# Optimization experiments

Hardware: AMD Instinct MI355X
Metric: run time of the kernel (lower is better)

## Reference

```python
import jax, jax.numpy as jnp
import numpy as np

B, D, P = 1024, 1024, 16  # batch, latent_dim(=out_dim), part_dim

def setup_inputs() -> dict:
    key = jax.random.key(0)
    k1, k2 = jax.random.split(key)
    x = jax.random.normal(k1, (B, D, P), dtype=jnp.float32)
    # per-part Linear weights, torch Linear weight shape [out, in] stacked over parts
    W = jax.random.normal(k2, (P, D, D), dtype=jnp.float32) * 0.02
    return {"x": x, "W": W}

def reference(x, W):
    # x: [B, D, P]; W: [P, O, D] (O == D here). stack_dim=-1: slice last dim,
    # apply part-specific Linear (no bias) + exact GELU, stack on last dim.
    y = jnp.einsum('bdp,pod->bop', x, W)  # grouped per-part GEMM -> [B, O, P]
    return jax.nn.gelu(y, approximate=False)
```

## Files before the change

### kernel.cpp

```cpp
#include <hip/hip_runtime.h>
#include <hip/hip_bf16.h>
#include <math.h>

typedef __hip_bfloat16 bf16;
typedef __attribute__((ext_vector_type(8))) short bf16x8;
typedef __attribute__((ext_vector_type(4))) float f32x4;

#define DI static __device__ __forceinline__

constexpr int NB = 1024;
constexpr int ND = 1024;
constexpr int NP = 16;
constexpr int BKT = 32;
constexpr int NKT = ND / BKT;
constexpr int LDP = 1032;

DI float gelu_exact(float x) {
    return 0.5f * x * (1.0f + erff(x * 0.70710678118654752f));
}

DI ushort bf16_bits(float f) {
    bf16 h = __float2bfloat16(f);
    return *reinterpret_cast<ushort*>(&h);
}

__global__ __launch_bounds__(256) void pack_kernel(const float* __restrict__ x,
                                                   const float* __restrict__ w,
                                                   bf16* __restrict__ xp,
                                                   bf16* __restrict__ wp) {
    __shared__ ushort lds[16][LDP];
    if (blockIdx.x < NB) {
        const int b = blockIdx.x;
        const int t = threadIdx.x;
        const float* xb = x + (size_t)b * (ND * NP);
#pragma unroll
        for (int it = 0; it < 8; ++it) {
            const int u  = it * 256 + t;
            const int dh = u >> 2;
            const int p0 = (u & 3) * 4;
            const float4 va = *reinterpret_cast<const float4*>(&xb[(size_t)(dh * 2)     * NP + p0]);
            const float4 vb = *reinterpret_cast<const float4*>(&xb[(size_t)(dh * 2 + 1) * NP + p0]);
            const float a0[4] = { va.x, va.y, va.z, va.w };
            const float a1[4] = { vb.x, vb.y, vb.z, vb.w };
#pragma unroll
            for (int k = 0; k < 4; ++k) {
                const uint packed = (uint)bf16_bits(a0[k]) | ((uint)bf16_bits(a1[k]) << 16);
                *reinterpret_cast<uint*>(&lds[p0 + k][dh * 2]) = packed;
            }
        }
        __syncthreads();
        const int p = threadIdx.x >> 4, j = threadIdx.x & 15;
        bf16* dst = xp + (size_t)p * (NB * ND) + (size_t)b * ND;
#pragma unroll
        for (int it = 0; it < 8; ++it) {
            const int c = it * 16 + j;
            *reinterpret_cast<bf16x8*>(&dst[c * 8]) =
                *reinterpret_cast<const bf16x8*>(&lds[p][c * 8]);
        }
    } else {
        const size_t i = ((size_t)(blockIdx.x - NB) * 256 + threadIdx.x) * 8;
        const float4 f0 = *reinterpret_cast<const float4*>(&w[i]);
        const float4 f1 = *reinterpret_cast<const float4*>(&w[i + 4]);
        alignas(16) bf16 tmp[8] = { __float2bfloat16(f0.x), __float2bfloat16(f0.y),
                                    __float2bfloat16(f0.z), __float2bfloat16(f0.w),
                                    __float2bfloat16(f1.x), __float2bfloat16(f1.y),
                                    __float2bfloat16(f1.z), __float2bfloat16(f1.w) };
        *reinterpret_cast<bf16x8*>(&wp[i]) = *reinterpret_cast<const bf16x8*>(tmp);
    }
}

__global__ __launch_bounds__(512, 2) void gemm8_kernel(const bf16* __restrict__ xp,
                                                       const bf16* __restrict__ wp,
                                                       bf16* __restrict__ y) {
    __shared__ bf16 As[3][256 * BKT];
    __shared__ bf16 Bs[3][256 * BKT];
    const int i = blockIdx.x;
    const int p    = ((i & 7) << 1) | ((i >> 3) & 1);
    const int tile = i >> 4;
    const int bt = (tile >> 2) * 256;
    const int ot = (tile & 3) * 256;
    const bf16* A  = xp + (size_t)p * NB * ND;
    const bf16* Bm = wp + (size_t)p * ND * ND;
    const int t = threadIdx.x;
    const int l = t & 63, w = t >> 6;
    const int wr = w >> 2, wc = w & 3;
    const int lr = l & 15, g = l >> 4;

    f32x4 acc[8][4] = {};

    auto stage = [&](int buf, int kt, int q) {
        const int s   = ((q & 1) * 8 + w) * 64 + l;
        const int row = s >> 2;
        const int cb  = (s & 3) ^ (row & 3);
        const bf16* gsrc = (q < 2 ? A + (size_t)(bt + row) * ND
                                  : Bm + (size_t)(ot + row) * ND) + kt * BKT + cb * 8;
        bf16* ldst = (q < 2 ? &As[buf][((q & 1) * 8 + w) * 512]
                            : &Bs[buf][((q & 1) * 8 + w) * 512]);
        __builtin_amdgcn_global_load_lds((const __attribute__((address_space(1))) void*)gsrc,
                                         (__attribute__((address_space(3))) void*)ldst, 16, 0, 0);
    };
    auto readA = [&](int buf, int m) -> bf16x8 {
        const int row  = wr * 128 + m * 16 + lr;
        const int slot = row * 4 + (g ^ (row & 3));
        return *reinterpret_cast<const bf16x8*>(&As[buf][slot * 8]);
    };
    auto readB = [&](int buf, int n) -> bf16x8 {
        const int row  = wc * 64 + n * 16 + lr;
        const int slot = row * 4 + (g ^ (row & 3));
        return *reinterpret_cast<const bf16x8*>(&Bs[buf][slot * 8]);
    };

#pragma unroll
    for (int q = 0; q < 4; ++q) stage(0, 0, q);
#pragma unroll
    for (int q = 0; q < 4; ++q) stage(1, 1, q);
    asm volatile("s_waitcnt vmcnt(4)" ::: "memory");
    __builtin_amdgcn_s_barrier();
    __builtin_amdgcn_sched_barrier(0);

    int bufc = 0, bufs = 2;
#pragma unroll 1
    for (int kt = 0; kt < NKT; ++kt) {
        bf16x8 bfr[4], af[4];
#pragma unroll
        for (int n = 0; n < 4; ++n) bfr[n] = readB(bufc, n);
#pragma unroll
        for (int m = 0; m < 4; ++m) af[m] = readA(bufc, m);
        if (kt + 2 < NKT) { stage(bufs, kt + 2, 0); stage(bufs, kt + 2, 1); }
        __builtin_amdgcn_s_barrier();
        asm volatile("s_waitcnt lgkmcnt(0)" ::: "memory");
        __builtin_amdgcn_s_setprio(1);
#pragma unroll
        for (int m = 0; m < 4; ++m)
#pragma unroll
            for (int n = 0; n < 4; ++n)
                acc[m][n] = __builtin_amdgcn_mfma_f32_16x16x32_bf16(af[m], bfr[n], acc[m][n], 0, 0, 0);
        __builtin_amdgcn_s_setprio(0);
        __builtin_amdgcn_s_barrier();
#pragma unroll
        for (int m = 0; m < 4; ++m) af[m] = readA(bufc, 4 + m);
        if (kt + 2 < NKT) { stage(bufs, kt + 2, 2); stage(bufs, kt + 2, 3); }
        __builtin_amdgcn_s_barrier();
        asm volatile("s_waitcnt lgkmcnt(0)" ::: "memory");
        __builtin_amdgcn_s_setprio(1);
#pragma unroll
        for (int m = 0; m < 4; ++m)
#pragma unroll
            for (int n = 0; n < 4; ++n)
                acc[4 + m][n] = __builtin_amdgcn_mfma_f32_16x16x32_bf16(af[m], bfr[n], acc[4 + m][n], 0, 0, 0);
        __builtin_amdgcn_s_setprio(0);
        if (kt < NKT - 1) {
            if (kt + 2 < NKT) asm volatile("s_waitcnt vmcnt(4)" ::: "memory");
            else              asm volatile("s_waitcnt vmcnt(0)" ::: "memory");
            __builtin_amdgcn_s_barrier();
            __builtin_amdgcn_sched_barrier(0);
        }
        bufc = (bufc == 2) ? 0 : bufc + 1;
        bufs = (bufs == 2) ? 0 : bufs + 1;
    }

    const int r4 = (l >> 4) * 4, lc = l & 15;
    bf16* yp = y + (size_t)p * NB * ND;
#pragma unroll
    for (int m = 0; m < 8; ++m) {
#pragma unroll
        for (int j = 0; j < 4; ++j) {
            const int row = bt + wr * 128 + m * 16 + r4 + j;
#pragma unroll
            for (int n = 0; n < 4; ++n) {
                const int col = ot + wc * 64 + n * 16 + lc;
                yp[(size_t)row * ND + col] = __float2bfloat16(gelu_exact(acc[m][n][j]));
            }
        }
    }
}

__global__ __launch_bounds__(256) void unpack_kernel(const bf16* __restrict__ y,
                                                     float* __restrict__ out) {
    const size_t gidx = (size_t)blockIdx.x * 256 + threadIdx.x;
    const size_t o = gidx & 1023;
    const size_t b = gidx >> 10;
    const bf16* yb = y + b * (size_t)ND + o;
    float v[16];
#pragma unroll
    for (int p = 0; p < 16; ++p)
        v[p] = __bfloat162float(yb[(size_t)p * (NB * ND)]);
    float4* dst = reinterpret_cast<float4*>(out + gidx * NP);
#pragma unroll
    for (int q = 0; q < 4; ++q)
        dst[q] = make_float4(v[q * 4], v[q * 4 + 1], v[q * 4 + 2], v[q * 4 + 3]);
}

__global__ __launch_bounds__(256, 4) void gemm_direct_kernel(const bf16* __restrict__ xp,
                                                             const bf16* __restrict__ wp,
                                                             float* __restrict__ out) {
    constexpr int BK = 32;
    __shared__ bf16 As[2][128 * BK];
    __shared__ bf16 Bs[2][128 * BK];
    const int i = blockIdx.x;
    const int p    = ((i & 7) << 1) | ((i >> 9) & 1);
    const int tile = (i >> 3) & 63;
    const int ot = (tile & 7) * 128;
    const int bt = (tile >> 3) * 128;
    const bf16* A  = xp + (size_t)p * NB * ND;
    const bf16* Bm = wp + (size_t)p * ND * ND;
    const int t = threadIdx.x;
    const int l = t & 63;
    const int w = t >> 6;
    const int wr = w >> 1, wc = w & 1;
    f32x4 acc[4][4] = {};
    auto stage = [&](int buf, int k0) {
#pragma unroll
        for (int r = 0; r < 2; ++r) {
            const int c   = r * 256 + t;
            const int row = c >> 2;
            const int cc  = c & 3;
            const bf16* ga = A  + (size_t)(bt + row) * ND + (k0 + cc * 8);
            const bf16* gb = Bm + (size_t)(ot + row) * ND + (k0 + cc * 8);
            bf16* la = &As[buf][(r * 256 + w * 64) * 8];
            bf16* lb = &Bs[buf][(r * 256 + w * 64) * 8];
            __builtin_amdgcn_global_load_lds((const __attribute__((address_space(1))) void*)ga,
                                             (__attribute__((address_space(3))) void*)la, 16, 0, 0);
            __builtin_amdgcn_global_load_lds((const __attribute__((address_space(1))) void*)gb,
                                             (__attribute__((address_space(3))) void*)lb, 16, 0, 0);
        }
    };
    int buf = 0;
    stage(0, 0);
    for (int kt = 0; kt < ND / BK; ++kt) {
        __syncthreads();
        if (kt + 1 < ND / BK) stage(buf ^ 1, (kt + 1) * BK);
        const int lr = l & 15;
        const int lk = (l >> 4) * 8;
        bf16x8 af[4], bfr[4];
#pragma unroll
        for (int m = 0; m < 4; ++m)
            af[m] = *reinterpret_cast<const bf16x8*>(&As[buf][(wr * 64 + m * 16 + lr) * BK + lk]);
#pragma unroll
        for (int n = 0; n < 4; ++n)
            bfr[n] = *reinterpret_cast<const bf16x8*>(&Bs[buf][(wc * 64 + n * 16 + lr) * BK + lk]);
#pragma unroll
        for (int m = 0; m < 4; ++m)
#pragma unroll
            for (int n = 0; n < 4; ++n)
                acc[m][n] = __builtin_amdgcn_mfma_f32_16x16x32_bf16(af[m], bfr[n], acc[m][n], 0, 0, 0);
        buf ^= 1;
    }
    const int lr4 = (l >> 4) * 4;
    const int lc  = l & 15;
    const int row0 = bt + wr * 64, col0 = ot + wc * 64;
#pragma unroll
    for (int m = 0; m < 4; ++m)
#pragma unroll
        for (int j = 0; j < 4; ++j) {
            const int r = row0 + m * 16 + lr4 + j;
#pragma unroll
            for (int n = 0; n < 4; ++n) {
                const int c = col0 + n * 16 + lc;
                out[((size_t)r * ND + c) * NP + p] = gelu_exact(acc[m][n][j]);
            }
        }
}

__global__ __launch_bounds__(256) void fallback_kernel(const float* __restrict__ x,
                                                       const float* __restrict__ w,
                                                       float* __restrict__ out) {
    __shared__ float As[64][17];
    __shared__ float Bs[64][17];
    const int p = blockIdx.z, bt = blockIdx.y * 64, ot = blockIdx.x * 64;
    const int t = threadIdx.x;
    const int tx = t & 15, ty = t >> 4;
    float acc[4][4] = {};
    for (int k0 = 0; k0 < ND; k0 += 16) {
        __syncthreads();
#pragma unroll
        for (int i = 0; i < 4; ++i) {
            const int idx = i * 256 + t;
            const int r = idx >> 4, k = idx & 15;
            As[r][k] = x[((size_t)(bt + r) * ND + k0 + k) * NP + p];
            Bs[r][k] = w[(size_t)p * ND * ND + (size_t)(ot + r) * ND + k0 + k];
        }
        __syncthreads();
#pragma unroll
        for (int k = 0; k < 16; ++k) {
            float a[4], bb[4];
#pragma unroll
            for (int i = 0; i < 4; ++i) a[i] = As[ty * 4 + i][k];
#pragma unroll
            for (int j = 0; j < 4; ++j) bb[j] = Bs[tx * 4 + j][k];
#pragma unroll
            for (int i = 0; i < 4; ++i)
#pragma unroll
                for (int j = 0; j < 4; ++j) acc[i][j] += a[i] * bb[j];
        }
    }
#pragma unroll
    for (int i = 0; i < 4; ++i)
#pragma unroll
        for (int j = 0; j < 4; ++j)
            out[((size_t)(bt + ty * 4 + i) * ND + (ot + tx * 4 + j)) * NP + p] =
                gelu_exact(acc[i][j]);
}

extern "C" void kernel_launch(void* const* d_in, const int* in_sizes, int n_in,
                              void* d_out, int out_size, void* d_ws, size_t ws_size,
                              hipStream_t stream) {
    const float* x = (const float*)d_in[0];
    const float* w = (const float*)d_in[1];
    float* out = (float*)d_out;

    const size_t nElem     = (size_t)NP * NB * ND;
    const size_t packBytes = nElem * sizeof(bf16) * 2;
    const size_t yBytes    = nElem * sizeof(bf16);

    if (ws_size >= packBytes) {
        bf16* xp = (bf16*)d_ws;
        bf16* wp = xp + nElem;
        pack_kernel<<<NB + (int)(nElem / (256 * 8)), 256, 0, stream>>>(x, w, xp, wp);
        if (ws_size >= packBytes + yBytes) {
            bf16* y = (bf16*)((char*)d_ws + packBytes);
            gemm8_kernel<<<256, 512, 0, stream>>>(xp, wp, y);
            unpack_kernel<<<(int)(NB * ND / 256), 256, 0, stream>>>(y, out);
        } else {
            gemm_direct_kernel<<<1024, 256, 0, stream>>>(xp, wp, out);
        }
    } else {
        fallback_kernel<<<dim3(16, 16, 16), 256, 0, stream>>>(x, w, out);
    }
}
```

Before: 114.7 us.

## Switch gemm8 to 32x32x16 MFMA tiles and move GELU into unpack

Replaces the 16x16x32 bf16 MFMA tiling in the 256x256 GEMM kernel with 32x32x16 MFMA, changing accumulators to f32x16, the LDS read pattern and the swizzle. Each K-step now reloads B fragments for both halves. The GELU is moved from the GEMM epilogue into the unpack kernel, so the intermediate is stored pre-activation in bf16. This aims for higher MFMA throughput and fewer LDS reads per FLOP, and takes erf work out of the GEMM tail, at the cost of a different layout and swizzle that must stay correct.

After: 110.6 us. 1.04x faster.

```diff
diff --git a/kernel.cpp b/kernel.cpp
--- a/kernel.cpp
+++ b/kernel.cpp
@@ -5,6 +5,7 @@
 typedef __hip_bfloat16 bf16;
 typedef __attribute__((ext_vector_type(8))) short bf16x8;
 typedef __attribute__((ext_vector_type(4))) float f32x4;
+typedef __attribute__((ext_vector_type(16))) float f32x16;
 
 #define DI static __device__ __forceinline__
 
@@ -84,14 +85,14 @@
     const int t = threadIdx.x;
     const int l = t & 63, w = t >> 6;
     const int wr = w >> 2, wc = w & 3;
-    const int lr = l & 15, g = l >> 4;
-
-    f32x4 acc[8][4] = {};
+    const int lr32 = l & 31, g2 = l >> 5;
+
+    f32x16 acc[4][2] = {};
 
     auto stage = [&](int buf, int kt, int q) {
         const int s   = ((q & 1) * 8 + w) * 64 + l;
         const int row = s >> 2;
-        const int cb  = (s & 3) ^ (row & 3);
+        const int cb  = (s & 3) ^ ((row >> 1) & 3);
         const bf16* gsrc = (q < 2 ? A + (size_t)(bt + row) * ND
                                   : Bm + (size_t)(ot + row) * ND) + kt * BKT + cb * 8;
         bf16* ldst = (q < 2 ? &As[buf][((q & 1) * 8 + w) * 512]
@@ -99,14 +100,16 @@
         __builtin_amdgcn_global_load_lds((const __attribute__((address_space(1))) void*)gsrc,
                                          (__attribute__((address_space(3))) void*)ldst, 16, 0, 0);
     };
-    auto readA = [&](int buf, int m) -> bf16x8 {
-        const int row  = wr * 128 + m * 16 + lr;
-        const int slot = row * 4 + (g ^ (row & 3));
+    auto readA = [&](int buf, int m, int s) -> bf16x8 {
+        const int row  = wr * 128 + m * 32 + lr32;
+        const int ch   = s * 2 + g2;
+        const int slot = row * 4 + (ch ^ ((row >> 1) & 3));
         return *reinterpret_cast<const bf16x8*>(&As[buf][slot * 8]);
     };
-    auto readB = [&](int buf, int n) -> bf16x8 {
-        const int row  = wc * 64 + n * 16 + lr;
-        const int slot = row * 4 + (g ^ (row & 3));
+    auto readB = [&](int buf, int n, int s) -> bf16x8 {
+        const int row  = wc * 64 + n * 32 + lr32;
+        const int ch   = s * 2 + g2;
+        const int slot = row * 4 + (ch ^ ((row >> 1) & 3));
         return *reinterpret_cast<const bf16x8*>(&Bs[buf][slot * 8]);
     };
 
@@ -121,11 +124,11 @@
     int bufc = 0, bufs = 2;
 #pragma unroll 1
     for (int kt = 0; kt < NKT; ++kt) {
-        bf16x8 bfr[4], af[4];
-#pragma unroll
-        for (int n = 0; n < 4; ++n) bfr[n] = readB(bufc, n);
-#pragma unroll
-        for (int m = 0; m < 4; ++m) af[m] = readA(bufc, m);
+        bf16x8 bfr[2], af[4];
+#pragma unroll
+        for (int n = 0; n < 2; ++n) bfr[n] = readB(bufc, n, 0);
+#pragma unroll
+        for (int m = 0; m < 4; ++m) af[m] = readA(bufc, m, 0);
         if (kt + 2 < NKT) { stage(bufs, kt + 2, 0); stage(bufs, kt + 2, 1); }
         __builtin_amdgcn_s_barrier();
         asm volatile("s_waitcnt lgkmcnt(0)" ::: "memory");
@@ -133,12 +136,14 @@
 #pragma unroll
         for (int m = 0; m < 4; ++m)
 #pragma unroll
-            for (int n = 0; n < 4; ++n)
-                acc[m][n] = __builtin_amdgcn_mfma_f32_16x16x32_bf16(af[m], bfr[n], acc[m][n], 0, 0, 0);
+            for (int n = 0; n < 2; ++n)
+                acc[m][n] = __builtin_amdgcn_mfma_f32_32x32x16_bf16(af[m], bfr[n], acc[m][n], 0, 0, 0);
         __builtin_amdgcn_s_setprio(0);
         __builtin_amdgcn_s_barrier();
 #pragma unroll
-        for (int m = 0; m < 4; ++m) af[m] = readA(bufc, 4 + m);
+        for (int n = 0; n < 2; ++n) bfr[n] = readB(bufc, n, 1);
+#pragma unroll
+        for (int m = 0; m < 4; ++m) af[m] = readA(bufc, m, 1);
         if (kt + 2 < NKT) { stage(bufs, kt + 2, 2); stage(bufs, kt + 2, 3); }
         __builtin_amdgcn_s_barrier();
         asm volatile("s_waitcnt lgkmcnt(0)" ::: "memory");
@@ -146,8 +151,8 @@
 #pragma unroll
         for (int m = 0; m < 4; ++m)
 #pragma unroll
-            for (int n = 0; n < 4; ++n)
-                acc[4 + m][n] = __builtin_amdgcn_mfma_f32_16x16x32_bf16(af[m], bfr[n], acc[4 + m][n], 0, 0, 0);
+            for (int n = 0; n < 2; ++n)
+                acc[m][n] = __builtin_amdgcn_mfma_f32_32x32x16_bf16(af[m], bfr[n], acc[m][n], 0, 0, 0);
         __builtin_amdgcn_s_setprio(0);
         if (kt < NKT - 1) {
             if (kt + 2 < NKT) asm volatile("s_waitcnt vmcnt(4)" ::: "memory");
@@ -159,17 +164,16 @@
         bufs = (bufs == 2) ? 0 : bufs + 1;
     }
 
-    const int r4 = (l >> 4) * 4, lc = l & 15;
     bf16* yp = y + (size_t)p * NB * ND;
 #pragma unroll
-    for (int m = 0; m < 8; ++m) {
-#pragma unroll
-        for (int j = 0; j < 4; ++j) {
-            const int row = bt + wr * 128 + m * 16 + r4 + j;
-#pragma unroll
-            for (int n = 0; n < 4; ++n) {
-                const int col = ot + wc * 64 + n * 16 + lc;
-                yp[(size_t)row * ND + col] = __float2bfloat16(gelu_exact(acc[m][n][j]));
+    for (int m = 0; m < 4; ++m) {
+#pragma unroll
+        for (int n = 0; n < 2; ++n) {
+#pragma unroll
+            for (int reg = 0; reg < 16; ++reg) {
+                const int row = bt + wr * 128 + m * 32 + (reg & 3) + 8 * (reg >> 2) + 4 * g2;
+                const int col = ot + wc * 64 + n * 32 + lr32;
+                yp[(size_t)row * ND + col] = __float2bfloat16(acc[m][n][reg]);
             }
         }
     }
@@ -184,7 +188,7 @@
     float v[16];
 #pragma unroll
     for (int p = 0; p < 16; ++p)
-        v[p] = __bfloat162float(yb[(size_t)p * (NB * ND)]);
+        v[p] = gelu_exact(__bfloat162float(yb[(size_t)p * (NB * ND)]));
     float4* dst = reinterpret_cast<float4*>(out + gidx * NP);
 #pragma unroll
     for (int q = 0; q < 4; ++q)
```
